# Kernel optimization log

Hardware: AMD Instinct MI355X
Metric: run time of the kernel (lower is better)

## Reference

```python
import jax, jax.numpy as jnp
import numpy as np
from jax.scipy.special import logsumexp

B, N, D, NUM_CLASSES = 8192, 8192, 256, 64
TEMPERATURE = 1.0


def setup_inputs() -> dict:
    key = jax.random.key(0)
    k1, k2, k3, k4 = jax.random.split(key, 4)
    return {
        "text_features": jax.random.normal(k1, (B, D), dtype=jnp.float32),
        "image_features": jax.random.normal(k2, (N, D), dtype=jnp.float32),
        "t_label": jax.random.randint(k3, (B,), 0, NUM_CLASSES),
        "i_targets": jax.random.randint(k4, (N,), 0, NUM_CLASSES),
    }


def reference(text_features, image_features, t_label, i_targets):
    # logits[i,j] = <text_i, image_j> / T   -> [B, N]
    logits = jnp.matmul(text_features, image_features.T) / TEMPERATURE
    mask = t_label[:, None] == i_targets[None, :]  # [B, N] positives
    neg_inf = jnp.array(-jnp.inf, dtype=logits.dtype)
    # per-row logsumexp over positives of -logits, and over negatives of +logits
    lse_p = logsumexp(jnp.where(mask, -logits, neg_inf), axis=1)
    lse_n = logsumexp(jnp.where(mask, neg_inf, logits), axis=1)
    loss = jnp.mean(jax.nn.softplus(lse_n + lse_p))
    return loss
```

## Files before the change

kernel.cpp:

```cpp
#include <hip/hip_runtime.h>
#include <hip/hip_bf16.h>


#define B_ROWS   8192
#define N_COLS   8192
#define DIM      256
#define CSPLIT   32
#define NTILES   ((N_COLS / CSPLIT) / 32)
#define BLK_ROWS 128
#define THREADS  512

typedef __attribute__((ext_vector_type(8))) short bf16x8;
typedef __attribute__((ext_vector_type(4))) float f32x4;

#if __has_builtin(__builtin_amdgcn_exp2f)
#define EXP2F(x) __builtin_amdgcn_exp2f(x)
#else
#define EXP2F(x) exp2f(x)
#endif
#if __has_builtin(__builtin_amdgcn_logf)
#define LOG2F(x) __builtin_amdgcn_logf(x)
#else
#define LOG2F(x) log2f(x)
#endif

__device__ __forceinline__ unsigned short f2bf(float f) {
    union { float f; unsigned u; } c; c.f = f;
    return (unsigned short)((c.u + 0x7FFFu + ((c.u >> 16) & 1u)) >> 16);
}

__global__ void cvt_all_kernel(const float* __restrict__ text,
                               const float* __restrict__ img,
                               unsigned short* __restrict__ Abf,
                               unsigned short* __restrict__ Bt,
                               float* __restrict__ gsum) {
    const int i = blockIdx.x * blockDim.x + threadIdx.x;
    if (i < 4096) {
        reinterpret_cast<float4*>(gsum)[i] = float4{0.f, 0.f, 0.f, 0.f};
    }
    if (i < 262144) {
        const float4* src = reinterpret_cast<const float4*>(text) + i * 2;
        float4 v0 = src[0], v1 = src[1];
        unsigned short s[8];
        s[0] = f2bf(v0.x); s[1] = f2bf(v0.y); s[2] = f2bf(v0.z); s[3] = f2bf(v0.w);
        s[4] = f2bf(v1.x); s[5] = f2bf(v1.y); s[6] = f2bf(v1.z); s[7] = f2bf(v1.w);
        reinterpret_cast<bf16x8*>(Abf)[i] = *reinterpret_cast<const bf16x8*>(s);
    } else {
        const int C = i - 262144;
        const int g = C >> 10, c = C & 1023;
        const int col = g * 32 + (c & 31);
        const int k8  = c >> 5;
        const float4* src =
            reinterpret_cast<const float4*>(img + (size_t)col * DIM + k8 * 8);
        float4 v0 = src[0], v1 = src[1];
        unsigned short s[8];
        s[0] = f2bf(v0.x); s[1] = f2bf(v0.y); s[2] = f2bf(v0.z); s[3] = f2bf(v0.w);
        s[4] = f2bf(v1.x); s[5] = f2bf(v1.y); s[6] = f2bf(v1.z); s[7] = f2bf(v1.w);
        reinterpret_cast<bf16x8*>(Bt)[C] = *reinterpret_cast<const bf16x8*>(s);
    }
}

__launch_bounds__(THREADS, 4)
__global__ void fused_gemm_lse(const unsigned short* __restrict__ Abf,
                               const unsigned short* __restrict__ Bt,
                               const int* __restrict__ tlab,
                               const int* __restrict__ itgt,
                               float* __restrict__ gsum_p,
                               float* __restrict__ gsum_n) {
    __shared__ char lds[2 * 16384] __attribute__((aligned(128)));

    const int tid  = threadIdx.x;
    const int lane = tid & 63;
    const int wave = tid >> 6;
    const int l15  = lane & 15;
    const int q    = lane >> 4;
    const int rb   = blockIdx.x * BLK_ROWS + wave * 16;
    const int cb0  = blockIdx.y * (N_COLS / CSPLIT);

    bf16x8 afrag[8];
    const bf16x8* arow =
        reinterpret_cast<const bf16x8*>(Abf + (size_t)(rb + l15) * DIM) + q;
#pragma unroll
    for (int ks = 0; ks < 8; ++ks) afrag[ks] = arow[ks * 4];

    int rowcls[4];
#pragma unroll
    for (int j = 0; j < 4; ++j) rowcls[j] = tlab[rb + q * 4 + j];

    int ccls0[NTILES], ccls1[NTILES];
#pragma unroll
    for (int t = 0; t < NTILES; ++t) {
        ccls0[t] = itgt[cb0 + t * 32 + l15];
        ccls1[t] = itgt[cb0 + t * 32 + 16 + l15];
    }

    float sump[4] = {0.f, 0.f, 0.f, 0.f};
    float sumn[4] = {0.f, 0.f, 0.f, 0.f};

    const char* bsrc = (const char*)Bt
        + ((size_t)blockIdx.y * NTILES) * 16384 + tid * 16;
    char* ldsd = lds + tid * 16;

#define STAGE(T, BUF) do {                                                    \
    _Pragma("unroll")                                                         \
    for (int i_ = 0; i_ < 2; ++i_)                                            \
        __builtin_amdgcn_global_load_lds(                                     \
            (const __attribute__((address_space(1))) unsigned int*)           \
                (bsrc + (size_t)(T) * 16384 + i_ * 8192),                     \
            (__attribute__((address_space(3))) unsigned int*)                 \
                (ldsd + (BUF) * 16384 + i_ * 8192),                           \
            16, 0, 0);                                                        \
} while (0)

    const float L2E = 1.4426950408889634f;
    const float C2  = 72.0f;

    STAGE(0, 0);

#pragma unroll
    for (int t = 0; t < NTILES; ++t) {
        if (t + 1 < NTILES) {
            STAGE(t + 1, (t + 1) & 1);
            asm volatile("s_waitcnt vmcnt(2)" ::: "memory");
        } else {
            asm volatile("s_waitcnt vmcnt(0)" ::: "memory");
        }
        __builtin_amdgcn_s_barrier();
        __builtin_amdgcn_sched_barrier(0);

        f32x4 acc0 = {0.f, 0.f, 0.f, 0.f};
        f32x4 acc1 = {0.f, 0.f, 0.f, 0.f};
        const char* bb = lds + (t & 1) * 16384 + q * 512 + l15 * 16;
#pragma unroll
        for (int ks = 0; ks < 8; ++ks) {
            bf16x8 b0 = *reinterpret_cast<const bf16x8*>(bb + ks * 2048);
            bf16x8 b1 = *reinterpret_cast<const bf16x8*>(bb + ks * 2048 + 256);
            acc0 = __builtin_amdgcn_mfma_f32_16x16x32_bf16(afrag[ks], b0, acc0,
                                                           0, 0, 0);
            acc1 = __builtin_amdgcn_mfma_f32_16x16x32_bf16(afrag[ks], b1, acc1,
                                                           0, 0, 0);
        }
        __builtin_amdgcn_sched_barrier(0);
        __builtin_amdgcn_s_barrier();

        const int cc0 = ccls0[t], cc1 = ccls1[t];
#pragma unroll
        for (int j = 0; j < 4; ++j) {
            const float x0 = acc0[j];
            const bool  p0 = (rowcls[j] == cc0);
            const float e0 = EXP2F(__builtin_fmaf(x0, p0 ? -L2E : L2E, -C2));
            sump[j] += p0 ? e0 : 0.f;
            sumn[j] += p0 ? 0.f : e0;
            const float x1 = acc1[j];
            const bool  p1 = (rowcls[j] == cc1);
            const float e1 = EXP2F(__builtin_fmaf(x1, p1 ? -L2E : L2E, -C2));
            sump[j] += p1 ? e1 : 0.f;
            sumn[j] += p1 ? 0.f : e1;
        }
    }
#undef STAGE

#pragma unroll
    for (int j = 0; j < 4; ++j) {
        float vp = sump[j], vn = sumn[j];
#pragma unroll
        for (int m = 1; m < 16; m <<= 1) {
            vp += __shfl_xor(vp, m, 64);
            vn += __shfl_xor(vn, m, 64);
        }
        if (l15 == 0) {
            const int row = rb + q * 4 + j;
            atomicAdd(&gsum_p[row], vp);
            atomicAdd(&gsum_n[row], vn);
        }
    }
}

__global__ void finalize_kernel(const float* __restrict__ gsum_p,
                                const float* __restrict__ gsum_n,
                                float* __restrict__ out) {
    __shared__ float red[1024];
    const float LN2 = 0.6931471805599453f;
    const float C2  = 72.0f;
    float acc = 0.f;
    for (int i = threadIdx.x; i < B_ROWS; i += 1024) {
        float zp = (LOG2F(gsum_p[i]) + C2) * LN2;
        float zn = (LOG2F(gsum_n[i]) + C2) * LN2;
        float z  = zp + zn;
        float sp = fmaxf(z, 0.f) + log1pf(expf(-fabsf(z)));
        acc += sp;
    }
    red[threadIdx.x] = acc;
    __syncthreads();
    for (int s = 512; s > 0; s >>= 1) {
        if ((int)threadIdx.x < s) red[threadIdx.x] += red[threadIdx.x + s];
        __syncthreads();
    }
    if (threadIdx.x == 0) out[0] = red[0] / (float)B_ROWS;
}

extern "C" void kernel_launch(void* const* d_in, const int* in_sizes, int n_in,
                              void* d_out, int out_size, void* d_ws, size_t ws_size,
                              hipStream_t stream) {
    const float* text = (const float*)d_in[0];
    const float* img  = (const float*)d_in[1];
    const int* tlab   = (const int*)d_in[2];
    const int* itgt   = (const int*)d_in[3];
    float* out        = (float*)d_out;

    char* ws = (char*)d_ws;
    unsigned short* Abf = (unsigned short*)(ws);
    unsigned short* Bt  = (unsigned short*)(ws + (size_t)B_ROWS * DIM * 2);
    float* gsum_p = (float*)(ws + (size_t)(B_ROWS + N_COLS) * DIM * 2);
    float* gsum_n = gsum_p + B_ROWS;

    cvt_all_kernel<<<(2 * 262144) / 256, 256, 0, stream>>>(text, img, Abf, Bt,
                                                           gsum_p);

    dim3 grid(B_ROWS / BLK_ROWS, CSPLIT);
    fused_gemm_lse<<<grid, THREADS, 0, stream>>>(Abf, Bt, tlab, itgt,
                                                 gsum_p, gsum_n);

    finalize_kernel<<<1, 1024, 0, stream>>>(gsum_p, gsum_n, out);
}
```

Baseline: 70.95 us.

## Double rows per wave and single-buffer LDS with staging after compute

Each wave now computes 32 rows (two A fragments) against every B tile, doubling reuse of each LDS-staged B tile and halving the number of blocks that stream B. LDS drops to a single 16KB buffer. The next tile is loaded after the MFMAs, so its load overlaps only the exp/accumulate epilogue rather than the compute. Column-class loads also move from a fully unrolled register array to a per-iteration prefetch. In exchange, register pressure rises (launch bounds lowered to 2) and load/compute overlap is reduced.

```diff
diff --git a/kernel.cpp b/kernel.cpp
--- a/kernel.cpp
+++ b/kernel.cpp
@@ -7,7 +7,7 @@
 #define DIM      256
 #define CSPLIT   32
 #define NTILES   ((N_COLS / CSPLIT) / 32)
-#define BLK_ROWS 128
+#define BLK_ROWS 256
 #define THREADS  512
 
 typedef __attribute__((ext_vector_type(8))) short bf16x8;
@@ -60,118 +60,146 @@
     }
 }
 
-__launch_bounds__(THREADS, 4)
+__launch_bounds__(THREADS, 2)
 __global__ void fused_gemm_lse(const unsigned short* __restrict__ Abf,
                                const unsigned short* __restrict__ Bt,
                                const int* __restrict__ tlab,
                                const int* __restrict__ itgt,
                                float* __restrict__ gsum_p,
                                float* __restrict__ gsum_n) {
-    __shared__ char lds[2 * 16384] __attribute__((aligned(128)));
+    __shared__ char lds[16384] __attribute__((aligned(128)));
 
     const int tid  = threadIdx.x;
     const int lane = tid & 63;
     const int wave = tid >> 6;
     const int l15  = lane & 15;
     const int q    = lane >> 4;
-    const int rb   = blockIdx.x * BLK_ROWS + wave * 16;
+    const int rb   = blockIdx.x * BLK_ROWS + wave * 32;
     const int cb0  = blockIdx.y * (N_COLS / CSPLIT);
 
-    bf16x8 afrag[8];
-    const bf16x8* arow =
+    bf16x8 afrag0[8], afrag1[8];
+    const bf16x8* arow0 =
         reinterpret_cast<const bf16x8*>(Abf + (size_t)(rb + l15) * DIM) + q;
-#pragma unroll
-    for (int ks = 0; ks < 8; ++ks) afrag[ks] = arow[ks * 4];
-
-    int rowcls[4];
-#pragma unroll
-    for (int j = 0; j < 4; ++j) rowcls[j] = tlab[rb + q * 4 + j];
-
-    int ccls0[NTILES], ccls1[NTILES];
-#pragma unroll
-    for (int t = 0; t < NTILES; ++t) {
-        ccls0[t] = itgt[cb0 + t * 32 + l15];
-        ccls1[t] = itgt[cb0 + t * 32 + 16 + l15];
-    }
-
-    float sump[4] = {0.f, 0.f, 0.f, 0.f};
-    float sumn[4] = {0.f, 0.f, 0.f, 0.f};
+    const bf16x8* arow1 =
+        reinterpret_cast<const bf16x8*>(Abf + (size_t)(rb + 16 + l15) * DIM) + q;
+#pragma unroll
+    for (int ks = 0; ks < 8; ++ks) {
+        afrag0[ks] = arow0[ks * 4];
+        afrag1[ks] = arow1[ks * 4];
+    }
+
+    int rowcls0[4], rowcls1[4];
+#pragma unroll
+    for (int j = 0; j < 4; ++j) {
+        rowcls0[j] = tlab[rb + q * 4 + j];
+        rowcls1[j] = tlab[rb + 16 + q * 4 + j];
+    }
+
+    float sump0[4] = {0, 0, 0, 0}, sumn0[4] = {0, 0, 0, 0};
+    float sump1[4] = {0, 0, 0, 0}, sumn1[4] = {0, 0, 0, 0};
 
     const char* bsrc = (const char*)Bt
         + ((size_t)blockIdx.y * NTILES) * 16384 + tid * 16;
     char* ldsd = lds + tid * 16;
 
-#define STAGE(T, BUF) do {                                                    \
+#define STAGE(T) do {                                                         \
     _Pragma("unroll")                                                         \
     for (int i_ = 0; i_ < 2; ++i_)                                            \
         __builtin_amdgcn_global_load_lds(                                     \
             (const __attribute__((address_space(1))) unsigned int*)           \
                 (bsrc + (size_t)(T) * 16384 + i_ * 8192),                     \
             (__attribute__((address_space(3))) unsigned int*)                 \
-                (ldsd + (BUF) * 16384 + i_ * 8192),                           \
+                (ldsd + i_ * 8192),                                           \
             16, 0, 0);                                                        \
 } while (0)
 
     const float L2E = 1.4426950408889634f;
     const float C2  = 72.0f;
 
-    STAGE(0, 0);
-
-#pragma unroll
+    STAGE(0);
+    int cc0 = itgt[cb0 + l15];
+    int cc1 = itgt[cb0 + 16 + l15];
+
     for (int t = 0; t < NTILES; ++t) {
-        if (t + 1 < NTILES) {
-            STAGE(t + 1, (t + 1) & 1);
-            asm volatile("s_waitcnt vmcnt(2)" ::: "memory");
-        } else {
-            asm volatile("s_waitcnt vmcnt(0)" ::: "memory");
-        }
-        __builtin_amdgcn_s_barrier();
-        __builtin_amdgcn_sched_barrier(0);
-
-        f32x4 acc0 = {0.f, 0.f, 0.f, 0.f};
-        f32x4 acc1 = {0.f, 0.f, 0.f, 0.f};
-        const char* bb = lds + (t & 1) * 16384 + q * 512 + l15 * 16;
+        __syncthreads();
+
+        f32x4 acc00 = {0, 0, 0, 0}, acc01 = {0, 0, 0, 0};
+        f32x4 acc10 = {0, 0, 0, 0}, acc11 = {0, 0, 0, 0};
+        const char* bb = lds + q * 512 + l15 * 16;
 #pragma unroll
         for (int ks = 0; ks < 8; ++ks) {
             bf16x8 b0 = *reinterpret_cast<const bf16x8*>(bb + ks * 2048);
             bf16x8 b1 = *reinterpret_cast<const bf16x8*>(bb + ks * 2048 + 256);
-            acc0 = __builtin_amdgcn_mfma_f32_16x16x32_bf16(afrag[ks], b0, acc0,
-                                                           0, 0, 0);
-            acc1 = __builtin_amdgcn_mfma_f32_16x16x32_bf16(afrag[ks], b1, acc1,
-                                                           0, 0, 0);
-        }
-        __builtin_amdgcn_sched_barrier(0);
-        __builtin_amdgcn_s_barrier();
-
-        const int cc0 = ccls0[t], cc1 = ccls1[t];
+            acc00 = __builtin_amdgcn_mfma_f32_16x16x32_bf16(afrag0[ks], b0,
+                                                            acc00, 0, 0, 0);
+            acc01 = __builtin_amdgcn_mfma_f32_16x16x32_bf16(afrag0[ks], b1,
+                                                            acc01, 0, 0, 0);
+            acc10 = __builtin_amdgcn_mfma_f32_16x16x32_bf16(afrag1[ks], b0,
+                                                            acc10, 0, 0, 0);
+            acc11 = __builtin_amdgcn_mfma_f32_16x16x32_bf16(afrag1[ks], b1,
+                                                            acc11, 0, 0, 0);
+        }
+        __syncthreads();
+
+        if (t + 1 < NTILES) STAGE(t + 1);
+
+        const int ncc0 = (t + 1 < NTILES) ? itgt[cb0 + (t + 1) * 32 + l15] : 0;
+        const int ncc1 = (t + 1 < NTILES) ? itgt[cb0 + (t + 1) * 32 + 16 + l15] : 0;
+
 #pragma unroll
         for (int j = 0; j < 4; ++j) {
-            const float x0 = acc0[j];
-            const bool  p0 = (rowcls[j] == cc0);
-            const float e0 = EXP2F(__builtin_fmaf(x0, p0 ? -L2E : L2E, -C2));
-            sump[j] += p0 ? e0 : 0.f;
-            sumn[j] += p0 ? 0.f : e0;
-            const float x1 = acc1[j];
-            const bool  p1 = (rowcls[j] == cc1);
-            const float e1 = EXP2F(__builtin_fmaf(x1, p1 ? -L2E : L2E, -C2));
-            sump[j] += p1 ? e1 : 0.f;
-            sumn[j] += p1 ? 0.f : e1;
-        }
+            {
+                const float x = acc00[j];
+                const bool  p = (rowcls0[j] == cc0);
+                const float e = EXP2F(__builtin_fmaf(x, p ? -L2E : L2E, -C2));
+                sump0[j] += p ? e : 0.f;
+                sumn0[j] += p ? 0.f : e;
+            }
+            {
+                const float x = acc01[j];
+                const bool  p = (rowcls0[j] == cc1);
+                const float e = EXP2F(__builtin_fmaf(x, p ? -L2E : L2E, -C2));
+                sump0[j] += p ? e : 0.f;
+                sumn0[j] += p ? 0.f : e;
+            }
+            {
+                const float x = acc10[j];
+                const bool  p = (rowcls1[j] == cc0);
+                const float e = EXP2F(__builtin_fmaf(x, p ? -L2E : L2E, -C2));
+                sump1[j] += p ? e : 0.f;
+                sumn1[j] += p ? 0.f : e;
+            }
+            {
+                const float x = acc11[j];
+                const bool  p = (rowcls1[j] == cc1);
+                const float e = EXP2F(__builtin_fmaf(x, p ? -L2E : L2E, -C2));
+                sump1[j] += p ? e : 0.f;
+                sumn1[j] += p ? 0.f : e;
+            }
+        }
+        cc0 = ncc0;
+        cc1 = ncc1;
     }
 #undef STAGE
 
 #pragma unroll
     for (int j = 0; j < 4; ++j) {
-        float vp = sump[j], vn = sumn[j];
+        float vp0 = sump0[j], vn0 = sumn0[j];
+        float vp1 = sump1[j], vn1 = sumn1[j];
 #pragma unroll
         for (int m = 1; m < 16; m <<= 1) {
-            vp += __shfl_xor(vp, m, 64);
-            vn += __shfl_xor(vn, m, 64);
+            vp0 += __shfl_xor(vp0, m, 64);
+            vn0 += __shfl_xor(vn0, m, 64);
+            vp1 += __shfl_xor(vp1, m, 64);
+            vn1 += __shfl_xor(vn1, m, 64);
         }
         if (l15 == 0) {
-            const int row = rb + q * 4 + j;
-            atomicAdd(&gsum_p[row], vp);
-            atomicAdd(&gsum_n[row], vn);
+            const int row0 = rb + q * 4 + j;
+            atomicAdd(&gsum_p[row0], vp0);
+            atomicAdd(&gsum_n[row0], vn0);
+            const int row1 = rb + 16 + q * 4 + j;
+            atomicAdd(&gsum_p[row1], vp1);
+            atomicAdd(&gsum_n[row1], vn1);
         }
     }
 }
```

Measured after the change: 67.50 us. 4.9% less time.
